# Kernel optimization log

Hardware: AMD Instinct MI355X
Metric: run time of the kernel (lower is better)

## Reference

```python
import jax, jax.numpy as jnp
import numpy as np
import math

B, T, C = 4, 2048, 1024
NH = 16
HD = C // NH


def setup_inputs() -> dict:
    key = jax.random.key(0)
    ks = jax.random.split(key, 10)
    s = 0.02
    x = jax.random.normal(ks[0], (B, T, C), dtype=jnp.float32)
    W_qkv = jax.random.normal(ks[1], (C, 3 * C), dtype=jnp.float32) * s
    b_qkv = jnp.zeros((3 * C,), dtype=jnp.float32)
    W_proj = jax.random.normal(ks[2], (C, C), dtype=jnp.float32) * s
    b_proj = jnp.zeros((C,), dtype=jnp.float32)
    asym_mean, asym_std = 1.0, 0.7
    q_scale = jax.random.normal(ks[3], (NH, HD), dtype=jnp.float32) * asym_std + asym_mean
    q_bias = jax.random.normal(ks[4], (NH, HD), dtype=jnp.float32) * asym_std + asym_mean
    k_scale = jax.random.normal(ks[5], (NH, HD), dtype=jnp.float32) * asym_std + asym_mean
    k_bias = jax.random.normal(ks[6], (NH, HD), dtype=jnp.float32) * asym_std + asym_mean
    return {"x": x, "W_qkv": W_qkv, "b_qkv": b_qkv, "W_proj": W_proj,
            "b_proj": b_proj, "q_scale": q_scale, "q_bias": q_bias,
            "k_scale": k_scale, "k_bias": k_bias}


def reference(x, W_qkv, b_qkv, W_proj, b_proj, q_scale, q_bias, k_scale, k_bias):
    Bx, Tx, Cx = x.shape
    qkv = x @ W_qkv + b_qkv                       # [B,T,3C]
    q, k, v = jnp.split(qkv, 3, axis=-1)
    # [B,T,C] -> [B,NH,T,HD]
    reshape = lambda t: t.reshape(Bx, Tx, NH, HD).transpose(0, 2, 1, 3)
    q, k, v = reshape(q), reshape(k), reshape(v)
    # per-head affine scaling of Q/K
    q = q * q_scale[None, :, None, :] + q_bias[None, :, None, :]
    k = k * k_scale[None, :, None, :] + k_bias[None, :, None, :]
    scores = jnp.einsum('bhqd,bhkd->bhqk', q, k) / math.sqrt(HD)  # [B,NH,T,T]
    causal = jnp.tril(jnp.ones((Tx, Tx), dtype=bool))
    scores = jnp.where(causal[None, None], scores, -jnp.inf)
    att = jax.nn.softmax(scores, axis=-1)
    y = jnp.einsum('bhqk,bhkd->bhqd', att, v)     # [B,NH,T,HD]
    y = y.transpose(0, 2, 1, 3).reshape(Bx, Tx, Cx)
    return y @ W_proj + b_proj
```

## Files before the change

kernel.cpp:

```cpp
#include <hip/hip_runtime.h>
#include <hip/hip_bf16.h>

typedef unsigned short u16;
typedef __attribute__((ext_vector_type(8))) short short8;
typedef __attribute__((ext_vector_type(4))) float floatx4;

#define B_SZ 4
#define T_SZ 2048
#define C_SZ 1024
#define NH_SZ 16
#define HD_SZ 64
#define M_TOT 8192
#define K_DIM 1024

#define QSCALE 0.1803368801111204f

#define OFF_XB   ((size_t)16)
#define OFF_WQT  (OFF_XB + 8388608)
#define OFF_WPT  (OFF_WQT + 3145728)
#define OFF_PB   (OFF_WPT + 1048576)
#define OFF_Q    (OFF_PB + 8192)
#define OFF_K    (OFF_Q + 8388608)
#define OFF_V    (OFF_K + 8388608)
#define OFF_Y    (OFF_V + 8388608)
#define PB_BQKV  0
#define PB_BPROJ 3072
#define PB_QSC   4096
#define PB_QBI   5120
#define PB_KSC   6144
#define PB_KBI   7168

__device__ __forceinline__ float bf2f(u16 u) {
    return __uint_as_float(((unsigned)u) << 16);
}
__device__ __forceinline__ u16 f2bf(float f) {
    unsigned x = __float_as_uint(f);
    unsigned r = (x + 0x7fffu + ((x >> 16) & 1u)) >> 16;
    return (u16)r;
}
__device__ __forceinline__ u16 f2bf_fast(float f) {
    return (u16)((__float_as_uint(f) + 0x8000u) >> 16);
}
__device__ __forceinline__ unsigned cvt_pk_bf16(float lo, float hi) {
    unsigned r;
    asm("v_cvt_pk_bf16_f32 %0, %1, %2" : "=v"(r) : "v"(lo), "v"(hi));
    return r;
}
__device__ __forceinline__ void gl_lds16(const u16* g, u16* l) {
    __builtin_amdgcn_global_load_lds(
        (const __attribute__((address_space(1))) void*)g,
        (__attribute__((address_space(3))) void*)l, 16, 0, 0);
}
__device__ __forceinline__ int detect_isf(const u16* xx, int lane) {
    float v0 = fabsf(bf2f(xx[lane * 2]));
    float v1 = fabsf(bf2f(xx[lane * 2 + 1]));
    int b0 = (v0 > 1024.0f) || (v0 != 0.0f && v0 < 9.5367431640625e-7f);
    int b1 = (v1 > 1024.0f) || (v1 != 0.0f && v1 < 9.5367431640625e-7f);
    unsigned long long ba = __ballot(b0), bb = __ballot(b1);
    return (__popcll(ba) + __popcll(bb)) > 8;
}

__global__ __launch_bounds__(256) void prep_k(
        const void* __restrict__ x,
        const void* __restrict__ Wqkv, const void* __restrict__ Wproj,
        const void* __restrict__ bqkv, const void* __restrict__ bproj,
        const void* __restrict__ qsc, const void* __restrict__ qbi,
        const void* __restrict__ ksc, const void* __restrict__ kbi,
        u16* __restrict__ xb, u16* __restrict__ Wt_qkv,
        u16* __restrict__ Wt_proj, u16* __restrict__ pb,
        int* __restrict__ flag) {
    __shared__ u16 t[32][33];
    const int blk = blockIdx.x;
    const int isf = detect_isf((const u16*)x, threadIdx.x & 63);
    if (blk == 0 && threadIdx.x == 0) flag[0] = isf;
    if (blk < 8192) {
        const int i = blk * 256 + threadIdx.x;
        if (isf) {
            const float4 v = ((const float4*)x)[i];
            ushort4 o;
            o.x = f2bf(v.x); o.y = f2bf(v.y); o.z = f2bf(v.z); o.w = f2bf(v.w);
            ((ushort4*)xb)[i] = o;
        } else {
            ((ushort4*)xb)[i] = ((const ushort4*)x)[i];
        }
        return;
    }
    if (blk < 8200) {
        const int i4 = (blk - 8192) * 256 + threadIdx.x;
        if (i4 >= 2048) return;
        const int e = i4 * 4;
        const void* src; int off;
        if (e < 3072)      { src = bqkv;  off = e; }
        else if (e < 4096) { src = bproj; off = e - 3072; }
        else if (e < 5120) { src = qsc;   off = e - 4096; }
        else if (e < 6144) { src = qbi;   off = e - 5120; }
        else if (e < 7168) { src = ksc;   off = e - 6144; }
        else               { src = kbi;   off = e - 7168; }
        ushort4 o;
        if (isf) {
            const float4 v = *(const float4*)((const float*)src + off);
            o.x = f2bf(v.x); o.y = f2bf(v.y); o.z = f2bf(v.z); o.w = f2bf(v.w);
        } else {
            o = *(const ushort4*)((const u16*)src + off);
        }
        *(ushort4*)&pb[e] = o;
        return;
    }
    const void* in; u16* out; int R, C, idx;
    if (blk < 11272) { idx = blk - 8200;  in = Wqkv;  out = Wt_qkv;  R = 1024; C = 3072; }
    else             { idx = blk - 11272; in = Wproj; out = Wt_proj; R = 1024; C = 1024; }
    const int nbx = C >> 5;
    const int c0 = (idx % nbx) * 32, r0 = (idx / nbx) * 32;
    const int tx = threadIdx.x & 31, ty = threadIdx.x >> 5;
    for (int i = 0; i < 4; i++) {
        int r = ty + i * 8;
        size_t gi = (size_t)(r0 + r) * C + c0 + tx;
        t[r][tx] = isf ? f2bf(((const float*)in)[gi]) : ((const u16*)in)[gi];
    }
    __syncthreads();
    for (int i = 0; i < 4; i++) {
        int cr = ty + i * 8;
        out[(size_t)(c0 + cr) * R + r0 + tx] = t[tx][cr];
    }
}

#define QG_BM 256
#define QG_BN 192
#define QG_NT 16

__global__ __launch_bounds__(512, 2) void qkv_gemm(
        const u16* __restrict__ X, const u16* __restrict__ Wt,
        const u16* __restrict__ pb,
        u16* __restrict__ Qb, u16* __restrict__ Kb, u16* __restrict__ Vb) {
    __shared__ __align__(16) u16 As[2][QG_BM * 64];
    __shared__ __align__(16) u16 Bs[2][QG_BN * 64];
    const int wgid = (blockIdx.x & 7) * 64 + (blockIdx.x >> 3);
    const int bm = (wgid >> 4) * QG_BM, bn = (wgid & 15) * QG_BN;
    const int tid = threadIdx.x;
    const int lane = tid & 63, w = tid >> 6;
    const int quad = lane >> 4, l16 = lane & 15;
    const int wm = (w & 3) * 64;
    const int wn = (w >> 2) * 96;
    const int lrow = lane >> 3;
    const int lcol = ((lane & 7) ^ lrow) * 8;
    const int sl0 = ((0 + quad) ^ (l16 & 7)) * 8;
    const int sl1 = ((4 + quad) ^ (l16 & 7)) * 8;

#define QG_STAGE(slot, kt) do {                                                  \
        const int k0_ = (kt) * 64;                                               \
        _Pragma("unroll")                                                        \
        for (int j = 0; j < 4; j++) {                                            \
            const int rb = w * 32 + j * 8;                                       \
            gl_lds16(&X[(size_t)(bm + rb + lrow) * K_DIM + k0_ + lcol],          \
                     &As[slot][rb * 64]);                                        \
        }                                                                        \
        _Pragma("unroll")                                                        \
        for (int j = 0; j < 3; j++) {                                            \
            const int rb = w * 24 + j * 8;                                       \
            gl_lds16(&Wt[(size_t)(bn + rb + lrow) * K_DIM + k0_ + lcol],         \
                     &Bs[slot][rb * 64]);                                        \
        }                                                                        \
    } while (0)

    floatx4 acc[4][6];
#pragma unroll
    for (int mi = 0; mi < 4; mi++)
#pragma unroll
        for (int ni = 0; ni < 6; ni++) acc[mi][ni] = 0.f;

    QG_STAGE(0, 0);
    QG_STAGE(1, 1);
    asm volatile("s_waitcnt vmcnt(7)" ::: "memory");
    __builtin_amdgcn_s_barrier();

    for (int t = 0; t < QG_NT; ++t) {
        const int cur = t & 1;
        const u16* as = As[cur];
        const u16* bs = Bs[cur];
        short8 a[4], b[6];
#pragma unroll
        for (int mi = 0; mi < 4; mi++)
            a[mi] = *(const short8*)&as[(wm + mi * 16 + l16) * 64 + sl0];
#pragma unroll
        for (int ni = 0; ni < 6; ni++)
            b[ni] = *(const short8*)&bs[(wn + ni * 16 + l16) * 64 + sl0];
        __builtin_amdgcn_s_setprio(1);
#pragma unroll
        for (int mi = 0; mi < 4; mi++)
#pragma unroll
            for (int ni = 0; ni < 6; ni++)
                acc[mi][ni] = __builtin_amdgcn_mfma_f32_16x16x32_bf16(
                    a[mi], b[ni], acc[mi][ni], 0, 0, 0);
        __builtin_amdgcn_s_setprio(0);
#pragma unroll
        for (int mi = 0; mi < 4; mi++)
            a[mi] = *(const short8*)&as[(wm + mi * 16 + l16) * 64 + sl1];
#pragma unroll
        for (int ni = 0; ni < 6; ni++)
            b[ni] = *(const short8*)&bs[(wn + ni * 16 + l16) * 64 + sl1];
        asm volatile("s_waitcnt lgkmcnt(0)" ::: "memory");
        __builtin_amdgcn_s_barrier();
        if (t < QG_NT - 1) {
            const int tn = (t + 2 < QG_NT) ? t + 2 : QG_NT - 1;
            QG_STAGE(cur, tn);
        }
        __builtin_amdgcn_s_setprio(1);
#pragma unroll
        for (int mi = 0; mi < 4; mi++)
#pragma unroll
            for (int ni = 0; ni < 6; ni++)
                acc[mi][ni] = __builtin_amdgcn_mfma_f32_16x16x32_bf16(
                    a[mi], b[ni], acc[mi][ni], 0, 0, 0);
        __builtin_amdgcn_s_setprio(0);
        asm volatile("s_waitcnt vmcnt(7)" ::: "memory");
        __builtin_amdgcn_s_barrier();
    }
#undef QG_STAGE

    const int bb = bm >> 11;
    const int tbase = bm & 2047;
#pragma unroll
    for (int ni = 0; ni < 6; ni++) {
        const int col = bn + wn + ni * 16 + l16;
        const int sec = col >> 10;
        const int cmod = col & 1023;
        const int h = cmod >> 6, d = cmod & 63;
        const float bv = bf2f(pb[PB_BQKV + col]);
        if (sec == 2) {
#pragma unroll
            for (int mi = 0; mi < 4; mi++) {
                const int t0 = tbase + wm + mi * 16 + quad * 4;
                ushort4 pk;
                pk.x = f2bf(acc[mi][ni][0] + bv);
                pk.y = f2bf(acc[mi][ni][1] + bv);
                pk.z = f2bf(acc[mi][ni][2] + bv);
                pk.w = f2bf(acc[mi][ni][3] + bv);
                *(ushort4*)&Vb[(((size_t)(bb * NH_SZ + h)) * HD_SZ + d) * T_SZ + t0] = pk;
            }
        } else {
            float sA, sB;
            if (sec == 0) {
                sA = bf2f(pb[PB_QSC + h * 64 + d]) * QSCALE;
                sB = bf2f(pb[PB_QBI + h * 64 + d]) * QSCALE;
            } else {
                sA = bf2f(pb[PB_KSC + h * 64 + d]);
                sB = bf2f(pb[PB_KBI + h * 64 + d]);
            }
            u16* dstbuf = (sec == 0) ? Qb : Kb;
#pragma unroll
            for (int mi = 0; mi < 4; mi++)
#pragma unroll
                for (int r = 0; r < 4; r++) {
                    const int tt = tbase + wm + mi * 16 + quad * 4 + r;
                    float v = (acc[mi][ni][r] + bv) * sA + sB;
                    dstbuf[(((size_t)(bb * NH_SZ + h)) * T_SZ + tt) * HD_SZ + d] = f2bf(v);
                }
        }
    }
}

__global__ __launch_bounds__(512, 6) void attn_k(const u16* __restrict__ Qb,
                                                 const u16* __restrict__ Kb,
                                                 const u16* __restrict__ Vtg,
                                                 u16* __restrict__ Y) {
    __shared__ __align__(16) u16 Ks[2][64 * 64];
    __shared__ __align__(16) u16 Vs[2][64 * 64];
    __shared__ __align__(16) u16 Ps[8 * 16 * 72];
    const int blk = blockIdx.x;
    const int head = blk & 63;
    const int qt = 15 - (blk >> 6);
    const int b = head >> 4, h = head & 15;
    const int tid = threadIdx.x, lane = tid & 63, w = tid >> 6;
    const int quad = lane >> 4, l16 = lane & 15;
    const size_t qk_off = (size_t)head * (T_SZ * HD_SZ);
    const size_t v_off = (size_t)head * (HD_SZ * T_SZ);
    u16* psw = &Ps[w * 1152];
    const int lr = lane >> 3;
    const int lc = ((lane & 7) ^ lr) * 8;
    const int sl0 = ((quad) ^ (l16 & 7)) * 8;
    const int sl1 = ((4 + quad) ^ (l16 & 7)) * 8;

    short8 ones;
    for (int j = 0; j < 8; j++) ones[j] = (short)0x3F80;

    const int q0 = qt * 128;
    const int rbase = q0 + w * 16;
    const int q = rbase + l16;
    const int nt = (q0 >> 6) + 2;

    const short8 aq0 = *(const short8*)&Qb[qk_off + (size_t)q * HD_SZ + quad * 8];
    const short8 aq1 = *(const short8*)&Qb[qk_off + (size_t)q * HD_SZ + 32 + quad * 8];

    floatx4 o[4];
    for (int mi = 0; mi < 4; mi++) o[mi] = 0.f;
    float m_run = -1e30f, l_run = 0.f;

    gl_lds16(&Kb[qk_off + (size_t)(w * 8 + lr) * HD_SZ + lc], &Ks[0][w * 512]);
    gl_lds16(&Vtg[v_off + (size_t)(w * 8 + lr) * T_SZ + lc], &Vs[0][w * 512]);

    for (int t = 0; t < nt; ++t) {
        const int cur = t & 1;
        const int k0 = t * 64;
        if (t + 1 < nt) {
            const int kn = k0 + 64;
            gl_lds16(&Kb[qk_off + (size_t)(kn + w * 8 + lr) * HD_SZ + lc],
                     &Ks[cur ^ 1][w * 512]);
            gl_lds16(&Vtg[v_off + (size_t)(w * 8 + lr) * T_SZ + kn + lc],
                     &Vs[cur ^ 1][w * 512]);
            asm volatile("s_waitcnt vmcnt(2)" ::: "memory");
        } else {
            asm volatile("s_waitcnt vmcnt(0)" ::: "memory");
        }
        __builtin_amdgcn_s_barrier();

        if (k0 <= rbase + 15) {
            const u16* ks = Ks[cur];
            const u16* vs = Vs[cur];
            floatx4 s[4];
            for (int ni = 0; ni < 4; ni++) s[ni] = 0.f;
            __builtin_amdgcn_s_setprio(1);
            for (int ni = 0; ni < 4; ni++)
                s[ni] = __builtin_amdgcn_mfma_f32_16x16x32_bf16(
                    *(const short8*)&ks[(ni * 16 + l16) * 64 + sl0], aq0, s[ni], 0, 0, 0);
            for (int ni = 0; ni < 4; ni++)
                s[ni] = __builtin_amdgcn_mfma_f32_16x16x32_bf16(
                    *(const short8*)&ks[(ni * 16 + l16) * 64 + sl1], aq1, s[ni], 0, 0, 0);
            __builtin_amdgcn_s_setprio(0);

            if (k0 + 63 > rbase) {
                for (int ni = 0; ni < 4; ni++)
                    for (int r = 0; r < 4; r++) {
                        int key = k0 + ni * 16 + quad * 4 + r;
                        if (key > q) s[ni][r] = -1e30f;
                    }
            }

            float t0 = fmaxf(fmaxf(s[0][0], s[0][1]), s[0][2]);
            float t1 = fmaxf(fmaxf(s[0][3], s[1][0]), s[1][1]);
            float t2 = fmaxf(fmaxf(s[1][2], s[1][3]), s[2][0]);
            float t3 = fmaxf(fmaxf(s[2][1], s[2][2]), s[2][3]);
            float t4 = fmaxf(fmaxf(s[3][0], s[3][1]), s[3][2]);
            float mx = fmaxf(fmaxf(fmaxf(t0, t1), fmaxf(t2, t3)),
                             fmaxf(t4, s[3][3]));
            mx = fmaxf(mx, __shfl_xor(mx, 16, 64));
            mx = fmaxf(mx, __shfl_xor(mx, 32, 64));

            if (!__all(mx <= m_run + 8.0f)) {
                const float mnew = fmaxf(m_run, mx);
                const float alpha = exp2f(m_run - mnew);
                m_run = mnew;
                for (int mi = 0; mi < 4; mi++) o[mi] *= alpha;
                l_run *= alpha;
            }
            for (int ni = 0; ni < 4; ni++)
                for (int r = 0; r < 4; r++)
                    s[ni][r] = exp2f(s[ni][r] - m_run);

            for (int ni = 0; ni < 4; ni++) {
                uint2 pp;
                pp.x = cvt_pk_bf16(s[ni][0], s[ni][1]);
                pp.y = cvt_pk_bf16(s[ni][2], s[ni][3]);
                *(uint2*)&psw[l16 * 72 + ni * 16 + quad * 4] = pp;
            }

            floatx4 s4 = 0.f;
            __builtin_amdgcn_s_setprio(1);
            for (int kk = 0; kk < 64; kk += 32) {
                short8 pfr = *(const short8*)&psw[l16 * 72 + kk + quad * 8];
                const int vsl = (kk == 0) ? sl0 : sl1;
                s4 = __builtin_amdgcn_mfma_f32_16x16x32_bf16(ones, pfr, s4, 0, 0, 0);
                for (int mi = 0; mi < 4; mi++) {
                    short8 vfr = *(const short8*)&vs[(mi * 16 + l16) * 64 + vsl];
                    o[mi] = __builtin_amdgcn_mfma_f32_16x16x32_bf16(vfr, pfr, o[mi], 0, 0, 0);
                }
            }
            __builtin_amdgcn_s_setprio(0);
            l_run += s4[0];
        }
        asm volatile("s_waitcnt lgkmcnt(0)" ::: "memory");
        __builtin_amdgcn_s_barrier();
    }

    const float inv = 1.0f / l_run;
    u16* yrow = &Y[(((size_t)b * T_SZ + q) * NH_SZ + h) * HD_SZ];
    for (int mi = 0; mi < 4; mi++) {
        uint2 pk2;
        pk2.x = cvt_pk_bf16(o[mi][0] * inv, o[mi][1] * inv);
        pk2.y = cvt_pk_bf16(o[mi][2] * inv, o[mi][3] * inv);
        *(uint2*)&yrow[mi * 16 + quad * 4] = pk2;
    }
}

#define PG_NT 16

__global__ __launch_bounds__(512, 4) void proj_gemm(const u16* __restrict__ Yin,
                                                    const u16* __restrict__ Wt,
                                                    const u16* __restrict__ pb,
                                                    void* __restrict__ out,
                                                    const int* __restrict__ flag) {
    __shared__ __align__(16) u16 As[2][128 * 64];
    __shared__ __align__(16) u16 Bs[2][128 * 64];
    const int isf = flag[0];
    const int bm = blockIdx.y * 128, bn = blockIdx.x * 128;
    const int tid = threadIdx.x;
    const int lane = tid & 63, w = tid >> 6;
    const int quad = lane >> 4, l16 = lane & 15;
    const int wm = (w & 3) * 32, wn = (w >> 2) * 64;
    const int lrow = lane >> 3;
    const int lcol = ((lane & 7) ^ lrow) * 8;
    const int sl0 = ((0 + quad) ^ (l16 & 7)) * 8;
    const int sl1 = ((4 + quad) ^ (l16 & 7)) * 8;

#define PG_STAGE(slot, kt) do {                                                  \
        const int k0_ = (kt) * 64;                                               \
        _Pragma("unroll")                                                        \
        for (int j = 0; j < 2; j++) {                                            \
            const int rb = w * 16 + j * 8;                                       \
            gl_lds16(&Yin[(size_t)(bm + rb + lrow) * K_DIM + k0_ + lcol],        \
                     &As[slot][rb * 64]);                                        \
            gl_lds16(&Wt[(size_t)(bn + rb + lrow) * K_DIM + k0_ + lcol],         \
                     &Bs[slot][rb * 64]);                                        \
        }                                                                        \
    } while (0)

    floatx4 acc[2][4];
#pragma unroll
    for (int mi = 0; mi < 2; mi++)
#pragma unroll
        for (int ni = 0; ni < 4; ni++) acc[mi][ni] = 0.f;

    PG_STAGE(0, 0);
    PG_STAGE(1, 1);
    asm volatile("s_waitcnt vmcnt(4)" ::: "memory");
    __builtin_amdgcn_s_barrier();

    for (int t = 0; t < PG_NT; ++t) {
        const int cur = t & 1;
        const u16* as = As[cur];
        const u16* bs = Bs[cur];
        short8 a[2], b[4];
#pragma unroll
        for (int mi = 0; mi < 2; mi++)
            a[mi] = *(const short8*)&as[(wm + mi * 16 + l16) * 64 + sl0];
#pragma unroll
        for (int ni = 0; ni < 4; ni++)
            b[ni] = *(const short8*)&bs[(wn + ni * 16 + l16) * 64 + sl0];
        __builtin_amdgcn_s_setprio(1);
#pragma unroll
        for (int mi = 0; mi < 2; mi++)
#pragma unroll
            for (int ni = 0; ni < 4; ni++)
                acc[mi][ni] = __builtin_amdgcn_mfma_f32_16x16x32_bf16(
                    a[mi], b[ni], acc[mi][ni], 0, 0, 0);
        __builtin_amdgcn_s_setprio(0);
#pragma unroll
        for (int mi = 0; mi < 2; mi++)
            a[mi] = *(const short8*)&as[(wm + mi * 16 + l16) * 64 + sl1];
#pragma unroll
        for (int ni = 0; ni < 4; ni++)
            b[ni] = *(const short8*)&bs[(wn + ni * 16 + l16) * 64 + sl1];
        asm volatile("s_waitcnt lgkmcnt(0)" ::: "memory");
        __builtin_amdgcn_s_barrier();
        if (t < PG_NT - 1) {
            const int tn = (t + 2 < PG_NT) ? t + 2 : PG_NT - 1;
            PG_STAGE(cur, tn);
        }
        __builtin_amdgcn_s_setprio(1);
#pragma unroll
        for (int mi = 0; mi < 2; mi++)
#pragma unroll
            for (int ni = 0; ni < 4; ni++)
                acc[mi][ni] = __builtin_amdgcn_mfma_f32_16x16x32_bf16(
                    a[mi], b[ni], acc[mi][ni], 0, 0, 0);
        __builtin_amdgcn_s_setprio(0);
        asm volatile("s_waitcnt vmcnt(4)" ::: "memory");
        __builtin_amdgcn_s_barrier();
    }
#undef PG_STAGE

    for (int mi = 0; mi < 2; mi++) {
        for (int ni = 0; ni < 4; ni++) {
            const int col = bn + wn + ni * 16 + l16;
            const float bv = bf2f(pb[PB_BPROJ + col]);
            for (int r = 0; r < 4; r++) {
                const int row = bm + wm + mi * 16 + quad * 4 + r;
                const float v = acc[mi][ni][r] + bv;
                if (isf) ((float*)out)[(size_t)row * C_SZ + col] = v;
                else     ((u16*)out)[(size_t)row * C_SZ + col] = f2bf(v);
            }
        }
    }
}

extern "C" void kernel_launch(void* const* d_in, const int* in_sizes, int n_in,
                              void* d_out, int out_size, void* d_ws, size_t ws_size,
                              hipStream_t stream) {
    const void* x     = d_in[0];
    const void* Wqkv  = d_in[1];
    const void* bqkv  = d_in[2];
    const void* Wproj = d_in[3];
    const void* bproj = d_in[4];
    const void* qsc   = d_in[5];
    const void* qbi   = d_in[6];
    const void* ksc   = d_in[7];
    const void* kbi   = d_in[8];

    u16* ws = (u16*)d_ws;
    int* flag    = (int*)d_ws;
    u16* xb      = ws + OFF_XB;
    u16* Wt_qkv  = ws + OFF_WQT;
    u16* Wt_proj = ws + OFF_WPT;
    u16* pb      = ws + OFF_PB;
    u16* Qb      = ws + OFF_Q;
    u16* Kb      = ws + OFF_K;
    u16* Vb      = ws + OFF_V;
    u16* Yb      = ws + OFF_Y;

    prep_k<<<12296, 256, 0, stream>>>(x, Wqkv, Wproj, bqkv, bproj,
                                      qsc, qbi, ksc, kbi,
                                      xb, Wt_qkv, Wt_proj, pb, flag);
    qkv_gemm<<<dim3(512), 512, 0, stream>>>(xb, Wt_qkv, pb, Qb, Kb, Vb);
    attn_k<<<dim3(1024), 512, 0, stream>>>(Qb, Kb, Vb, Yb);
    proj_gemm<<<dim3(8, 64), 512, 0, stream>>>(Yb, Wt_proj, pb, d_out, flag);
}
```

Baseline: 277.3 us.

## Software-pipeline QK^T one tile ahead of softmax and PV in attention

Restructures the flash-attention loop so the S=QK^T MFMAs for tile t+1 are issued before the softmax and PV work for tile t. K is prefetched two tiles ahead and V one tile ahead, with the vmcnt waits adjusted to match. The row-sum accumulator is now kept in the MFMA output register across iterations instead of being reduced to a scalar each tile. This is meant to hide MFMA latency behind softmax math, at the cost of higher register pressure and a more complex buffer and wait scheme.

```diff
diff --git a/kernel.cpp b/kernel.cpp
--- a/kernel.cpp
+++ b/kernel.cpp
@@ -287,46 +287,69 @@
     const int rbase = q0 + w * 16;
     const int q = rbase + l16;
     const int nt = (q0 >> 6) + 2;
+    const int last = nt - 1;
 
     const short8 aq0 = *(const short8*)&Qb[qk_off + (size_t)q * HD_SZ + quad * 8];
     const short8 aq1 = *(const short8*)&Qb[qk_off + (size_t)q * HD_SZ + 32 + quad * 8];
 
     floatx4 o[4];
     for (int mi = 0; mi < 4; mi++) o[mi] = 0.f;
-    float m_run = -1e30f, l_run = 0.f;
+    floatx4 s4p = 0.f;
+    float m_run = -1e30f;
 
     gl_lds16(&Kb[qk_off + (size_t)(w * 8 + lr) * HD_SZ + lc], &Ks[0][w * 512]);
     gl_lds16(&Vtg[v_off + (size_t)(w * 8 + lr) * T_SZ + lc], &Vs[0][w * 512]);
+    if (last >= 1)
+        gl_lds16(&Kb[qk_off + (size_t)(64 + w * 8 + lr) * HD_SZ + lc], &Ks[1][w * 512]);
+    asm volatile("s_waitcnt vmcnt(1)" ::: "memory");
+    __builtin_amdgcn_s_barrier();
+
+    floatx4 s[4];
+    for (int ni = 0; ni < 4; ni++) s[ni] = 0.f;
+    for (int ni = 0; ni < 4; ni++)
+        s[ni] = __builtin_amdgcn_mfma_f32_16x16x32_bf16(
+            *(const short8*)&Ks[0][(ni * 16 + l16) * 64 + sl0], aq0, s[ni], 0, 0, 0);
+    for (int ni = 0; ni < 4; ni++)
+        s[ni] = __builtin_amdgcn_mfma_f32_16x16x32_bf16(
+            *(const short8*)&Ks[0][(ni * 16 + l16) * 64 + sl1], aq1, s[ni], 0, 0, 0);
 
     for (int t = 0; t < nt; ++t) {
         const int cur = t & 1;
-        const int k0 = t * 64;
-        if (t + 1 < nt) {
-            const int kn = k0 + 64;
-            gl_lds16(&Kb[qk_off + (size_t)(kn + w * 8 + lr) * HD_SZ + lc],
-                     &Ks[cur ^ 1][w * 512]);
-            gl_lds16(&Vtg[v_off + (size_t)(w * 8 + lr) * T_SZ + kn + lc],
+        asm volatile("s_waitcnt lgkmcnt(0)" ::: "memory");
+        __builtin_amdgcn_s_barrier();
+        int just = 0;
+        if (t + 2 <= last) {
+            gl_lds16(&Kb[qk_off + (size_t)((t + 2) * 64 + w * 8 + lr) * HD_SZ + lc],
+                     &Ks[cur][w * 512]);
+            just++;
+        }
+        if (t + 1 <= last) {
+            gl_lds16(&Vtg[v_off + (size_t)(w * 8 + lr) * T_SZ + (t + 1) * 64 + lc],
                      &Vs[cur ^ 1][w * 512]);
-            asm volatile("s_waitcnt vmcnt(2)" ::: "memory");
-        } else {
-            asm volatile("s_waitcnt vmcnt(0)" ::: "memory");
-        }
+            just++;
+        }
+        if (just == 2)      asm volatile("s_waitcnt vmcnt(2)" ::: "memory");
+        else if (just == 1) asm volatile("s_waitcnt vmcnt(1)" ::: "memory");
+        else                asm volatile("s_waitcnt vmcnt(0)" ::: "memory");
         __builtin_amdgcn_s_barrier();
 
-        if (k0 <= rbase + 15) {
-            const u16* ks = Ks[cur];
-            const u16* vs = Vs[cur];
-            floatx4 s[4];
-            for (int ni = 0; ni < 4; ni++) s[ni] = 0.f;
+        floatx4 sn[4];
+        if ((t + 1) * 64 <= rbase + 15) {
+            const u16* kn = Ks[cur ^ 1];
+            for (int ni = 0; ni < 4; ni++) sn[ni] = 0.f;
             __builtin_amdgcn_s_setprio(1);
             for (int ni = 0; ni < 4; ni++)
-                s[ni] = __builtin_amdgcn_mfma_f32_16x16x32_bf16(
-                    *(const short8*)&ks[(ni * 16 + l16) * 64 + sl0], aq0, s[ni], 0, 0, 0);
+                sn[ni] = __builtin_amdgcn_mfma_f32_16x16x32_bf16(
+                    *(const short8*)&kn[(ni * 16 + l16) * 64 + sl0], aq0, sn[ni], 0, 0, 0);
             for (int ni = 0; ni < 4; ni++)
-                s[ni] = __builtin_amdgcn_mfma_f32_16x16x32_bf16(
-                    *(const short8*)&ks[(ni * 16 + l16) * 64 + sl1], aq1, s[ni], 0, 0, 0);
+                sn[ni] = __builtin_amdgcn_mfma_f32_16x16x32_bf16(
+                    *(const short8*)&kn[(ni * 16 + l16) * 64 + sl1], aq1, sn[ni], 0, 0, 0);
             __builtin_amdgcn_s_setprio(0);
-
+        }
+
+        if (t * 64 <= rbase + 15) {
+            const int k0 = t * 64;
+            const u16* vs = Vs[cur];
             if (k0 + 63 > rbase) {
                 for (int ni = 0; ni < 4; ni++)
                     for (int r = 0; r < 4; r++) {
@@ -350,7 +373,7 @@
                 const float alpha = exp2f(m_run - mnew);
                 m_run = mnew;
                 for (int mi = 0; mi < 4; mi++) o[mi] *= alpha;
-                l_run *= alpha;
+                s4p *= alpha;
             }
             for (int ni = 0; ni < 4; ni++)
                 for (int r = 0; r < 4; r++)
@@ -363,25 +386,22 @@
                 *(uint2*)&psw[l16 * 72 + ni * 16 + quad * 4] = pp;
             }
 
-            floatx4 s4 = 0.f;
             __builtin_amdgcn_s_setprio(1);
             for (int kk = 0; kk < 64; kk += 32) {
                 short8 pfr = *(const short8*)&psw[l16 * 72 + kk + quad * 8];
                 const int vsl = (kk == 0) ? sl0 : sl1;
-                s4 = __builtin_amdgcn_mfma_f32_16x16x32_bf16(ones, pfr, s4, 0, 0, 0);
+                s4p = __builtin_amdgcn_mfma_f32_16x16x32_bf16(ones, pfr, s4p, 0, 0, 0);
                 for (int mi = 0; mi < 4; mi++) {
                     short8 vfr = *(const short8*)&vs[(mi * 16 + l16) * 64 + vsl];
                     o[mi] = __builtin_amdgcn_mfma_f32_16x16x32_bf16(vfr, pfr, o[mi], 0, 0, 0);
                 }
             }
             __builtin_amdgcn_s_setprio(0);
-            l_run += s4[0];
-        }
-        asm volatile("s_waitcnt lgkmcnt(0)" ::: "memory");
-        __builtin_amdgcn_s_barrier();
-    }
-
-    const float inv = 1.0f / l_run;
+        }
+        for (int ni = 0; ni < 4; ni++) s[ni] = sn[ni];
+    }
+
+    const float inv = 1.0f / s4p[0];
     u16* yrow = &Y[(((size_t)b * T_SZ + q) * NH_SZ + h) * HD_SZ];
     for (int mi = 0; mi < 4; mi++) {
         uint2 pk2;
```

Result: slower. 299.4 us (+8.0%).
